# Performance work log

Hardware: AMD Instinct MI355X
Metric: run time of the kernel (lower is better)

The kernel has to match this reference:

```python
import jax, jax.numpy as jnp
from jax import lax
import numpy as np

B, S, E, H2, V = 128, 256, 256, 256, 50000  # batch, subword seq len, emb dim, per-direction hidden, vocab


def _make_masks(rng):
    # random subword lengths, word-start (bmask) and word-end (fmask) masks with equal counts per row
    lengths = rng.integers(S // 2, S + 1, size=B)
    pos = np.arange(S)[None, :]
    valid = pos < lengths[:, None]
    starts = (rng.random((B, S)) < 0.33) & valid
    starts[:, 0] = True
    nxt = np.concatenate([starts[:, 1:], np.zeros((B, 1), bool)], axis=1)
    fmask = valid & (nxt | (pos == lengths[:, None] - 1))
    return valid, fmask, starts


def setup_inputs():
    rng = np.random.default_rng(0)
    valid, fmask, bmask = _make_masks(rng)
    sw_ids = rng.integers(1, V, size=(B, S)) * valid  # 0 = pad
    key = jax.random.key(0)
    ks = jax.random.split(key, 8)
    se = float(np.sqrt(3.0 / E))       # random_embedding scale
    sh = float(1.0 / np.sqrt(H2))      # pytorch LSTM init scale
    u = lambda k, shape, s: jax.random.uniform(k, shape, jnp.float32, -s, s)
    return {
        "sw_ids": jnp.asarray(sw_ids, jnp.int32),
        "fmasks": jnp.asarray(fmask, jnp.int32),
        "bmasks": jnp.asarray(bmask, jnp.int32),
        "emb_W": u(ks[0], (V, E), se),
        "W_ih_f": u(ks[1], (4 * H2, E), sh),
        "W_hh_f": u(ks[2], (4 * H2, H2), sh),
        "b_f": u(ks[3], (4 * H2,), sh),
        "W_ih_b": u(ks[4], (4 * H2, E), sh),
        "W_hh_b": u(ks[5], (4 * H2, H2), sh),
        "b_b": u(ks[6], (4 * H2,), sh),
    }


def _lstm(x, mask, Wih, Whh, b):
    # x: [B,S,E]; mask: [B,S] float. Matches packed LSTM: state frozen and output
    # zeroed at padded steps (pad_packed_sequence zero-pads). Gate order i,f,g,o.
    h0 = jnp.zeros((x.shape[0], Whh.shape[1]), x.dtype)

    def step(carry, inp):
        h, c = carry
        xt, mt = inp
        g = xt @ Wih.T + h @ Whh.T + b
        i, f, gg, o = jnp.split(g, 4, axis=-1)
        c_new = jax.nn.sigmoid(f) * c + jax.nn.sigmoid(i) * jnp.tanh(gg)
        h_new = jax.nn.sigmoid(o) * jnp.tanh(c_new)
        m = mt[:, None]
        h = jnp.where(m > 0, h_new, h)
        c = jnp.where(m > 0, c_new, c)
        return (h, c), h * m

    _, ys = lax.scan(step, (h0, h0), (x.transpose(1, 0, 2), mask.T))
    return ys.transpose(1, 0, 2)  # [B,S,H2]


def _select_pad(out, mask, out_len):
    # vectorized masked_select + pad_sequence: stable-sort moves mask==1 positions
    # (in original order) to the front of the time axis, then zero beyond out_len.
    gather = jnp.argsort(1 - mask, axis=1)  # stable -> selected positions first
    sel = jnp.take_along_axis(out, gather[:, :, None], axis=1)
    word_valid = jnp.arange(out.shape[1])[None, :] < out_len[:, None]
    return sel * word_valid[:, :, None].astype(out.dtype)


def reference(sw_ids, fmasks, bmasks, emb_W, W_ih_f, W_hh_f, b_f, W_ih_b, W_hh_b, b_b):
    lengths = (sw_ids != 0).sum(axis=1)
    perm = jnp.argsort(-lengths)  # stable descending, like torch sort(descending=True)
    ids = sw_ids[perm]
    fm = fmasks[perm]
    bm = bmasks[perm]
    valid = (ids != 0).astype(emb_W.dtype)
    embeds = emb_W[ids]  # dropout is identity at eval time
    f_out = _lstm(embeds, valid, W_ih_f, W_hh_f, b_f)
    # backward direction: reverse in time (padding leads but state stays zero under mask)
    b_out = _lstm(embeds[:, ::-1], valid[:, ::-1], W_ih_b, W_hh_b, b_b)[:, ::-1]
    out_len = fm.sum(axis=1)
    f_pad = _select_pad(f_out, fm, out_len)
    b_pad = _select_pad(b_out, bm, out_len)
    perm2 = jnp.argsort(-out_len)
    out = jnp.concatenate([f_pad[perm2], b_pad[perm2]], axis=2)  # [B, S, 2*H2]
    return out, out_len[perm2]
```

## Files before the change

### kernel.cpp

```cpp
#include <hip/hip_runtime.h>
#include <hip/hip_bf16.h>
#include <hip/hip_fp16.h>
#include <math.h>
#include <stdint.h>

#define BB 128
#define SS 256
#define EE 256
#define HH 256
#define G4 1024
#define OUT_HEAD (BB*SS*2*HH)
#define SE 0.10825317547305482f

#define P8_HH_F 0
#define P8_HH_B 65536
#define P8_IH_F 131072
#define P8_IH_B 196608
#define SC_OFF  (1024*1024)
#define INT_OFF (1280*1024)
#define GX_OFF  (4*1024*1024)

__device__ __forceinline__ float sigf(float x){ return 1.0f/(1.0f+__expf(-x)); }
__device__ __forceinline__ float tanhx(float x){
    float t = __expf(2.0f*x);
    return 1.0f - 2.0f/(t+1.0f);
}
__device__ __forceinline__ int dot4(uint32_t a, uint32_t b, int acc){
    return __builtin_amdgcn_sdot4((int)a, (int)b, acc, false);
}

__global__ __launch_bounds__(64) void pack8(const float* __restrict__ W,
    uint32_t* __restrict__ P8, float* __restrict__ SC){
    const int g = blockIdx.x, lane = threadIdx.x;
    float4 w4 = ((const float4*)(W + (size_t)g*EE))[lane];
    float m = fmaxf(fmaxf(fabsf(w4.x), fabsf(w4.y)), fmaxf(fabsf(w4.z), fabsf(w4.w)));
    for(int off=32; off; off>>=1) m = fmaxf(m, __shfl_xor(m, off));
    const float inv = (m > 0.f) ? 127.f/m : 0.f;
    int b0 = (int)rintf(w4.x*inv), b1 = (int)rintf(w4.y*inv);
    int b2 = (int)rintf(w4.z*inv), b3 = (int)rintf(w4.w*inv);
    uint32_t p = (uint32_t)(b0 & 0xff) | ((uint32_t)(b1 & 0xff) << 8) |
                 ((uint32_t)(b2 & 0xff) << 16) | ((uint32_t)(b3 & 0xff) << 24);
    P8[lane*G4 + g] = p;
    if(lane == 0) SC[g] = m / 127.f;
}

__global__ void prep(const int* __restrict__ sw, const int* __restrict__ fm,
                     const int* __restrict__ bm, int* __restrict__ wsI,
                     float* __restrict__ out_tail){
    __shared__ int len_s[BB], flen_s[BB], perm_s[BB], olp_s[BB];
    int b = threadIdx.x;
    int cnt = 0, fcnt = 0;
    for(int t=0;t<SS;t++){
        cnt  += (sw[b*SS+t] != 0);
        fcnt += fm[b*SS+t];
    }
    len_s[b] = cnt; flen_s[b] = fcnt;
    __syncthreads();
    int r = 0;
    for(int b2=0;b2<BB;b2++){
        int l2 = len_s[b2];
        r += (l2 > cnt) || (l2 == cnt && b2 < b);
    }
    perm_s[r] = b;
    __syncthreads();
    int orig = perm_s[b];
    olp_s[b] = flen_s[orig];
    wsI[0*BB + b] = orig;
    wsI[1*BB + b] = len_s[orig];
    __syncthreads();
    int v = olp_s[b];
    int q = 0;
    for(int r2=0;r2<BB;r2++){
        int v2 = olp_s[r2];
        q += (v2 > v) || (v2 == v && r2 < b);
    }
    wsI[2*BB + b] = q;
    wsI[3*BB + b] = v;
    out_tail[q] = (float)v;
    int* fdst = wsI + 4*BB;
    int* bdst = fdst + BB*SS;
    int fc = 0, bc = 0;
    for(int t=0;t<SS;t++){
        int fv = fm[orig*SS+t];
        fdst[b*SS+t] = (fv && fc < v) ? (q*SS + fc) : -1;
        fc += fv;
        int bv = bm[orig*SS+t];
        bdst[b*SS+t] = (bv && bc < v) ? (q*SS + bc) : -1;
        bc += bv;
    }
}

__global__ __launch_bounds__(1024)
__attribute__((amdgpu_waves_per_eu(4,4)))
void xg8(const int* __restrict__ sw,
    const float* __restrict__ emb, const float* __restrict__ b_f,
    const float* __restrict__ b_b, const uint32_t* __restrict__ wsU,
    const float* __restrict__ scl, const int* __restrict__ wsI,
    _Float16* __restrict__ gx){
    __shared__ int x8i[64];
    const int tid = threadIdx.x, r = blockIdx.x, dir = blockIdx.y;
    const uint32_t* P = wsU + (dir ? P8_IH_B : P8_IH_F);
    uint32_t w[64];
    #pragma unroll
    for(int j=0;j<64;j++) w[j] = P[j*G4 + tid];
    #pragma unroll
    for(int j=0;j<64;j++) asm volatile("" : "+v"(w[j]));
    const float cs = scl[(2 + dir)*G4 + tid] * (SE/127.f);
    const float bias = (dir ? b_b : b_f)[tid];
    const int orig = wsI[r], L = wsI[BB + r];
    const int* ids = sw + orig*SS;
    float xv = 0.f;
    if(tid < EE) xv = emb[(size_t)ids[0]*EE + tid];
    _Float16* gxr = gx + ((size_t)(dir*BB + r))*SS*G4;

    for(int t=0;t<L;t++){
        if(tid < EE) ((signed char*)x8i)[tid] = (signed char)(int)rintf(xv*(127.f/SE));
        __syncthreads();
        if(tid < EE && t+1 < L) xv = emb[(size_t)ids[t+1]*EE + tid];
        int acc0 = 0, acc1 = 0;
        const uint4* hp = (const uint4*)x8i;
        #pragma unroll
        for(int j=0;j<16;j++){
            uint4 hv = hp[j];
            acc0 = dot4(w[4*j+0], hv.x, acc0);
            acc1 = dot4(w[4*j+1], hv.y, acc1);
            acc0 = dot4(w[4*j+2], hv.z, acc0);
            acc1 = dot4(w[4*j+3], hv.w, acc1);
        }
        gxr[(size_t)t*G4 + tid] = (_Float16)(bias + (float)(acc0 + acc1)*cs);
        __syncthreads();
    }
}

__global__ __launch_bounds__(1024)
__attribute__((amdgpu_waves_per_eu(4,4)))
void rec8(const uint32_t* __restrict__ wsU,
    const float* __restrict__ scl, const int* __restrict__ wsI,
    const _Float16* __restrict__ gx, float* __restrict__ out){
    __shared__ int h8i[64];
    __shared__ float gfl[G4];
    const int tid = threadIdx.x, r = blockIdx.x, dir = blockIdx.y;
    const uint32_t* P = wsU + (dir ? P8_HH_B : P8_HH_F);
    uint32_t w[64];
    #pragma unroll
    for(int j=0;j<64;j++) w[j] = P[j*G4 + tid];
    #pragma unroll
    for(int j=0;j<64;j++) asm volatile("" : "+v"(w[j]));
    const float csh = scl[dir*G4 + tid] * (1.f/127.f);
    const int L = wsI[BB + r];
    const int* dstA = wsI + 4*BB + (dir ? BB*SS : 0) + r*SS;
    if(tid < 64) h8i[tid] = 0;
    float cst = 0.f;
    const _Float16* gxr = gx + ((size_t)(dir*BB + r))*SS*G4;
    const int t0 = dir ? L-1 : 0, stp = dir ? -1 : 1;
    _Float16 gv = gxr[(size_t)t0*G4 + tid];
    __syncthreads();

    for(int s=0;s<L;s++){
        const int t = t0 + s*stp;
        const float gxv = (float)gv;
        if(s+1 < L) gv = gxr[(size_t)(t+stp)*G4 + tid];
        int acc0 = 0, acc1 = 0;
        const uint4* hp = (const uint4*)h8i;
        #pragma unroll
        for(int j=0;j<16;j++){
            uint4 hv = hp[j];
            acc0 = dot4(w[4*j+0], hv.x, acc0);
            acc1 = dot4(w[4*j+1], hv.y, acc1);
            acc0 = dot4(w[4*j+2], hv.z, acc0);
            acc1 = dot4(w[4*j+3], hv.w, acc1);
        }
        gfl[tid] = gxv + (float)(acc0 + acc1)*csh;
        __syncthreads();
        if(tid < HH){
            float gi = gfl[tid], gf = gfl[tid+256], gz = gfl[tid+512], go = gfl[tid+768];
            float i = sigf(gi), f = sigf(gf), z = tanhx(gz), o = sigf(go);
            cst = f*cst + i*z;
            float hn = o*tanhx(cst);
            ((signed char*)h8i)[tid] = (signed char)(int)rintf(hn*127.f);
            int dst = dstA[t];
            if(dst >= 0) out[(size_t)dst*(2*HH) + dir*HH + tid] = hn;
        }
        __syncthreads();
    }
}

extern "C" void kernel_launch(void* const* d_in, const int* in_sizes, int n_in,
                              void* d_out, int out_size, void* d_ws, size_t ws_size,
                              hipStream_t stream){
    const int*   sw    = (const int*)d_in[0];
    const int*   fm    = (const int*)d_in[1];
    const int*   bm    = (const int*)d_in[2];
    const float* emb   = (const float*)d_in[3];
    const float* Wih_f = (const float*)d_in[4];
    const float* Whh_f = (const float*)d_in[5];
    const float* b_f   = (const float*)d_in[6];
    const float* Wih_b = (const float*)d_in[7];
    const float* Whh_b = (const float*)d_in[8];
    const float* b_b   = (const float*)d_in[9];
    float* out = (float*)d_out;
    uint32_t* wsU = (uint32_t*)d_ws;
    float* scl = (float*)((char*)d_ws + SC_OFF);
    int* wsI = (int*)((char*)d_ws + INT_OFF);
    _Float16* gxp = (_Float16*)((char*)d_ws + GX_OFF);

    hipMemsetAsync(d_out, 0, (size_t)out_size*4, stream);
    pack8<<<G4, 64, 0, stream>>>(Whh_f, wsU + P8_HH_F, scl + 0*G4);
    pack8<<<G4, 64, 0, stream>>>(Whh_b, wsU + P8_HH_B, scl + 1*G4);
    pack8<<<G4, 64, 0, stream>>>(Wih_f, wsU + P8_IH_F, scl + 2*G4);
    pack8<<<G4, 64, 0, stream>>>(Wih_b, wsU + P8_IH_B, scl + 3*G4);
    prep<<<1, BB, 0, stream>>>(sw, fm, bm, wsI, out + OUT_HEAD);
    xg8<<<dim3(BB,2), 1024, 0, stream>>>(sw, emb, b_f, b_b, wsU, scl, wsI, gxp);
    rec8<<<dim3(BB,2), 1024, 0, stream>>>(wsU, scl, wsI, gxp, out);
}
```

Baseline: 533.0 us.

## Tile input projection as blocked int8 GEMM and split recurrent weights LDS/global

The input-gate kernel now quantizes 64 tokens at a time into a transposed shared tile. Each thread computes an 8-gate by 8-token int8 dot-product block, removing the per-token barrier loop and weight-in-register design. The recurrent kernel stores half of each thread's packed Whh row in swizzled shared memory and reloads the other half from global memory every timestep, freeing registers. That reload adds memory traffic on the serial recurrence path.

```diff
diff --git a/kernel.cpp b/kernel.cpp
--- a/kernel.cpp
+++ b/kernel.cpp
@@ -19,6 +19,8 @@
 #define SC_OFF  (1024*1024)
 #define INT_OFF (1280*1024)
 #define GX_OFF  (4*1024*1024)
+
+typedef _Float16 h8v __attribute__((ext_vector_type(8)));
 
 __device__ __forceinline__ float sigf(float x){ return 1.0f/(1.0f+__expf(-x)); }
 __device__ __forceinline__ float tanhx(float x){
@@ -92,60 +94,91 @@
 
 __global__ __launch_bounds__(1024)
 __attribute__((amdgpu_waves_per_eu(4,4)))
-void xg8(const int* __restrict__ sw,
-    const float* __restrict__ emb, const float* __restrict__ b_f,
-    const float* __restrict__ b_b, const uint32_t* __restrict__ wsU,
-    const float* __restrict__ scl, const int* __restrict__ wsI,
-    _Float16* __restrict__ gx){
-    __shared__ int x8i[64];
+void xg8g(const int* __restrict__ sw, const float* __restrict__ emb,
+    const float* __restrict__ b_f, const float* __restrict__ b_b,
+    const uint32_t* __restrict__ wsU, const float* __restrict__ scl,
+    const int* __restrict__ wsI, _Float16* __restrict__ gx){
+    __shared__ __align__(16) uint32_t xqT[64*64];
     const int tid = threadIdx.x, r = blockIdx.x, dir = blockIdx.y;
     const uint32_t* P = wsU + (dir ? P8_IH_B : P8_IH_F);
-    uint32_t w[64];
-    #pragma unroll
-    for(int j=0;j<64;j++) w[j] = P[j*G4 + tid];
-    #pragma unroll
-    for(int j=0;j<64;j++) asm volatile("" : "+v"(w[j]));
-    const float cs = scl[(2 + dir)*G4 + tid] * (SE/127.f);
-    const float bias = (dir ? b_b : b_f)[tid];
+    const int gt = tid & 127;
+    const int tt = tid >> 7;
     const int orig = wsI[r], L = wsI[BB + r];
     const int* ids = sw + orig*SS;
-    float xv = 0.f;
-    if(tid < EE) xv = emb[(size_t)ids[0]*EE + tid];
     _Float16* gxr = gx + ((size_t)(dir*BB + r))*SS*G4;
-
-    for(int t=0;t<L;t++){
-        if(tid < EE) ((signed char*)x8i)[tid] = (signed char)(int)rintf(xv*(127.f/SE));
-        __syncthreads();
-        if(tid < EE && t+1 < L) xv = emb[(size_t)ids[t+1]*EE + tid];
-        int acc0 = 0, acc1 = 0;
-        const uint4* hp = (const uint4*)x8i;
-        #pragma unroll
-        for(int j=0;j<16;j++){
-            uint4 hv = hp[j];
-            acc0 = dot4(w[4*j+0], hv.x, acc0);
-            acc1 = dot4(w[4*j+1], hv.y, acc1);
-            acc0 = dot4(w[4*j+2], hv.z, acc0);
-            acc1 = dot4(w[4*j+3], hv.w, acc1);
-        }
-        gxr[(size_t)t*G4 + tid] = (_Float16)(bias + (float)(acc0 + acc1)*cs);
+    const float* bias = dir ? b_b : b_f;
+    const float* scA = scl + (2+dir)*G4;
+    float bs[8], cs[8];
+    #pragma unroll
+    for(int k=0;k<8;k++){ bs[k] = bias[gt*8+k]; cs[k] = scA[gt*8+k]*(SE/127.f); }
+    const int qtok = tid & 63, qg = tid >> 6;
+
+    for(int t0 = 0; t0 < L; t0 += 64){
+        int tq = t0 + qtok;
+        #pragma unroll
+        for(int q=0;q<4;q++){
+            int d = qg + q*16;
+            uint32_t pv = 0u;
+            if(tq < L){
+                float4 xf = ((const float4*)(emb + (size_t)ids[tq]*EE))[d];
+                int b0=(int)rintf(xf.x*(127.f/SE)), b1=(int)rintf(xf.y*(127.f/SE));
+                int b2=(int)rintf(xf.z*(127.f/SE)), b3=(int)rintf(xf.w*(127.f/SE));
+                pv = (uint32_t)(b0 & 0xff) | ((uint32_t)(b1 & 0xff) << 8) |
+                     ((uint32_t)(b2 & 0xff) << 16) | ((uint32_t)(b3 & 0xff) << 24);
+            }
+            xqT[d*64 + qtok] = pv;
+        }
+        __syncthreads();
+
+        int acc[8][8];
+        #pragma unroll
+        for(int g=0;g<8;g++)
+            #pragma unroll
+            for(int k=0;k<8;k++) acc[g][k] = 0;
+
+        #pragma unroll 2
+        for(int j=0;j<64;j++){
+            uint32_t wv[8], xv[8];
+            *(uint4*)&wv[0] = *(const uint4*)&P[j*G4 + gt*8];
+            *(uint4*)&wv[4] = *(const uint4*)&P[j*G4 + gt*8 + 4];
+            *(uint4*)&xv[0] = *(const uint4*)&xqT[j*64 + tt*8];
+            *(uint4*)&xv[4] = *(const uint4*)&xqT[j*64 + tt*8 + 4];
+            #pragma unroll
+            for(int g=0;g<8;g++)
+                #pragma unroll
+                for(int k=0;k<8;k++)
+                    acc[g][k] = dot4(wv[g], xv[k], acc[g][k]);
+        }
+
+        #pragma unroll
+        for(int k=0;k<8;k++){
+            int t = t0 + tt*8 + k;
+            if(t < L){
+                h8v hv;
+                #pragma unroll
+                for(int g=0;g<8;g++) hv[g] = (_Float16)(bs[g] + (float)acc[g][k]*cs[g]);
+                *((h8v*)(gxr + (size_t)t*G4 + gt*8)) = hv;
+            }
+        }
         __syncthreads();
     }
 }
 
 __global__ __launch_bounds__(1024)
 __attribute__((amdgpu_waves_per_eu(4,4)))
-void rec8(const uint32_t* __restrict__ wsU,
-    const float* __restrict__ scl, const int* __restrict__ wsI,
-    const _Float16* __restrict__ gx, float* __restrict__ out){
+void rec8L(const uint32_t* __restrict__ wsU, const float* __restrict__ scl,
+    const int* __restrict__ wsI, const _Float16* __restrict__ gx,
+    float* __restrict__ out){
+    __shared__ __align__(16) uint32_t WC[32*1024];
+    __shared__ float gfl[G4];
     __shared__ int h8i[64];
-    __shared__ float gfl[G4];
     const int tid = threadIdx.x, r = blockIdx.x, dir = blockIdx.y;
     const uint32_t* P = wsU + (dir ? P8_HH_B : P8_HH_F);
-    uint32_t w[64];
     #pragma unroll
-    for(int j=0;j<64;j++) w[j] = P[j*G4 + tid];
-    #pragma unroll
-    for(int j=0;j<64;j++) asm volatile("" : "+v"(w[j]));
+    for(int j=0;j<32;j++){
+        uint32_t v = P[j*G4 + tid];
+        WC[tid*32 + (((j>>2) ^ (tid&7))<<2) + (j&3)] = v;
+    }
     const float csh = scl[dir*G4 + tid] * (1.f/127.f);
     const int L = wsI[BB + r];
     const int* dstA = wsI + 4*BB + (dir ? BB*SS : 0) + r*SS;
@@ -160,15 +193,30 @@
         const int t = t0 + s*stp;
         const float gxv = (float)gv;
         if(s+1 < L) gv = gxr[(size_t)(t+stp)*G4 + tid];
+        uint32_t ws[32];
+        #pragma unroll
+        for(int m=0;m<32;m++) ws[m] = P[(32+m)*G4 + tid];
+        uint32_t wc[32];
+        #pragma unroll
+        for(int jg=0;jg<8;jg++)
+            *(uint4*)&wc[jg*4] = *(const uint4*)&WC[tid*32 + ((jg ^ (tid&7))<<2)];
         int acc0 = 0, acc1 = 0;
         const uint4* hp = (const uint4*)h8i;
         #pragma unroll
-        for(int j=0;j<16;j++){
-            uint4 hv = hp[j];
-            acc0 = dot4(w[4*j+0], hv.x, acc0);
-            acc1 = dot4(w[4*j+1], hv.y, acc1);
-            acc0 = dot4(w[4*j+2], hv.z, acc0);
-            acc1 = dot4(w[4*j+3], hv.w, acc1);
+        for(int q=0;q<8;q++){
+            uint4 hv = hp[q];
+            acc0 = dot4(wc[q*4+0], hv.x, acc0);
+            acc1 = dot4(wc[q*4+1], hv.y, acc1);
+            acc0 = dot4(wc[q*4+2], hv.z, acc0);
+            acc1 = dot4(wc[q*4+3], hv.w, acc1);
+        }
+        #pragma unroll
+        for(int q=0;q<8;q++){
+            uint4 hv = hp[8+q];
+            acc0 = dot4(ws[q*4+0], hv.x, acc0);
+            acc1 = dot4(ws[q*4+1], hv.y, acc1);
+            acc0 = dot4(ws[q*4+2], hv.z, acc0);
+            acc1 = dot4(ws[q*4+3], hv.w, acc1);
         }
         gfl[tid] = gxv + (float)(acc0 + acc1)*csh;
         __syncthreads();
@@ -210,6 +258,6 @@
     pack8<<<G4, 64, 0, stream>>>(Wih_f, wsU + P8_IH_F, scl + 2*G4);
     pack8<<<G4, 64, 0, stream>>>(Wih_b, wsU + P8_IH_B, scl + 3*G4);
     prep<<<1, BB, 0, stream>>>(sw, fm, bm, wsI, out + OUT_HEAD);
-    xg8<<<dim3(BB,2), 1024, 0, stream>>>(sw, emb, b_f, b_b, wsU, scl, wsI, gxp);
-    rec8<<<dim3(BB,2), 1024, 0, stream>>>(wsU, scl, wsI, gxp, out);
-}
+    xg8g<<<dim3(BB,2), 1024, 0, stream>>>(sw, emb, b_f, b_b, wsU, scl, wsI, gxp);
+    rec8L<<<dim3(BB,2), 1024, 0, stream>>>(wsU, scl, wsI, gxp, out);
+}
```

New measurement: 596.6 us. +11.9%, slower.
